# Performance work log

Hardware: AMD Instinct MI355X
Metric: run time of the kernel (lower is better)

Reference implementation:

```python
import jax, jax.numpy as jnp
import numpy as np

SDIM, EDIM, HID, DEPTH = 128, 128, 64, 4
CUTOFF, EPS = 5.0, 1e-6
N, E = 40000, 512000
MSG_IN = 2 * SDIM + EDIM + 2   # [s_src, s_dst, e, dist, ea_d]
SCAL_IN = SDIM + HID


def silu(x):
    return x * jax.nn.sigmoid(x)


def setup_inputs() -> dict:
    key = jax.random.key(0)
    ks = jax.random.split(key, 16)

    def w(k, shape, fan):
        return jax.random.normal(k, shape, jnp.float32) / np.float32(np.sqrt(fan))

    return {
        "s": jax.random.normal(ks[0], (N, SDIM), jnp.float32),
        "v": jax.random.normal(ks[1], (N, 3), jnp.float32),
        "e": jax.random.normal(ks[2], (E, EDIM), jnp.float32),
        "edge_index": jax.random.randint(ks[3], (2, E), 0, N),
        "ea_d": jax.random.uniform(ks[4], (E, 1), dtype=jnp.float32),
        "ea_r": jax.random.normal(ks[5], (E, 3), jnp.float32),
        "batch": jnp.zeros((N,), jnp.int32),
        "We1": w(ks[6], (DEPTH, MSG_IN, HID), MSG_IN),
        "be1": jnp.zeros((DEPTH, HID), jnp.float32),
        "We2": w(ks[7], (DEPTH, HID, HID), HID),
        "be2": jnp.zeros((DEPTH, HID), jnp.float32),
        "Weo": w(ks[8], (DEPTH, HID, EDIM), HID),
        "beo": jnp.zeros((DEPTH, EDIM), jnp.float32),
        "Wv": w(ks[9], (DEPTH, HID, 1), HID),
        "bv": jnp.zeros((DEPTH, 1), jnp.float32),
        "Ws1": w(ks[10], (DEPTH, SCAL_IN, HID), SCAL_IN),
        "bs1": jnp.zeros((DEPTH, HID), jnp.float32),
        "Ws2": w(ks[11], (DEPTH, HID, SDIM), HID),
        "bs2": jnp.zeros((DEPTH, SDIM), jnp.float32),
    }


def egnn_forward(s, v, e, src, dst, ea_d,
                 We1, be1, We2, be2, Weo, beo, Wv, bv, Ws1, bs1, Ws2, bs2):
    n = s.shape[0]
    ne = e.shape[0]
    # mean aggregation: per-destination degree (clamped to 1)
    deg = jax.ops.segment_sum(jnp.ones((ne, 1), s.dtype), dst, num_segments=n)
    deg = jnp.maximum(deg, 1.0)
    for i in range(DEPTH):
        rel = v[src] - v[dst]                                          # [E,3]
        dist = jnp.sqrt(jnp.sum(rel * rel, axis=-1, keepdims=True) + EPS)  # [E,1]
        cw = 0.5 * (jnp.cos(jnp.pi * dist / CUTOFF) + 1.0) * (dist < CUTOFF)
        h = jnp.concatenate([s[src], s[dst], e, dist, ea_d], axis=-1)  # [E,MSG_IN]
        m = silu(silu(h @ We1[i] + be1[i]) @ We2[i] + be2[i]) * cw      # [E,HID]
        e = e + m @ Weo[i] + beo[i]                                    # edge residual
        wv = m @ Wv[i] + bv[i]                                         # [E,1]
        v = v + jax.ops.segment_sum(rel * wv, dst, num_segments=n) / deg
        agg = jax.ops.segment_sum(m, dst, num_segments=n) / deg        # [N,HID]
        s = s + silu(jnp.concatenate([s, agg], axis=-1) @ Ws1[i] + bs1[i]) @ Ws2[i] + bs2[i]
    return s, v, e


def reference(s, v, e, edge_index, ea_d, ea_r, batch,
              We1, be1, We2, be2, Weo, beo, Wv, bv, Ws1, bs1, Ws2, bs2):
    del batch, ea_r  # unused in the enhanced (EGCL_Edge_Fast) path
    src, dst = edge_index[0], edge_index[1]
    return egnn_forward(s, v, e, src, dst, ea_d,
                        We1, be1, We2, be2, Weo, beo, Wv, bv, Ws1, bs1, Ws2, bs2)
```

## Files before the change

### kernel.cpp

```cpp
#include <hip/hip_runtime.h>
#include <math.h>

#define N_NODES 40000
#define N_EDGES 512000
#define SDIM 128
#define EDIM 128
#define HID 64
#define DEPTH 4
#define MSG_IN 386
#define SCAL_IN 192
#define CUTOFF 5.0f
#define EPS_D 1e-6f

#define TILE_M 16
#define EW 8
#define ETHREADS 512
#define EBLOCKS 256
#define TWAVES (EBLOCKS * EW)
#define NTILES (N_EDGES / TILE_M)
#define ATILES (N_NODES / TILE_M)
#define SCAN_B 1024
#define SCAN_NB ((N_NODES + SCAN_B - 1) / SCAN_B)

typedef __attribute__((ext_vector_type(8))) short short8;
typedef __attribute__((ext_vector_type(4))) float f32x4;
typedef unsigned long long ull;

__device__ __forceinline__ float silu_f(float x) { return x / (1.0f + __expf(-x)); }

__device__ __forceinline__ unsigned short f2b(float x) {
  union { __bf16 b; unsigned short u; } v;
  v.b = (__bf16)x;
  return v.u;
}

__device__ __forceinline__ float b2f(unsigned short u) {
  union { unsigned int u32; float f; } v; v.u32 = (unsigned int)u << 16; return v.f;
}

__device__ __forceinline__ short8 pack8(f32x4 lo, f32x4 hi) {
  union { unsigned short u[8]; short8 s; } pk;
  pk.u[0] = f2b(lo[0]); pk.u[1] = f2b(lo[1]); pk.u[2] = f2b(lo[2]); pk.u[3] = f2b(lo[3]);
  pk.u[4] = f2b(hi[0]); pk.u[5] = f2b(hi[1]); pk.u[6] = f2b(hi[2]); pk.u[7] = f2b(hi[3]);
  return pk.s;
}

__global__ __launch_bounds__(256) void k_zero(float* __restrict__ p, int n) {
  int i = blockIdx.x * 256 + threadIdx.x;
  int stride = gridDim.x * 256;
  for (; i < n; i += stride) p[i] = 0.0f;
}

__global__ __launch_bounds__(256) void k_cnt(const int* __restrict__ dst,
                                             int* __restrict__ cnt, int ne) {
  int i = blockIdx.x * 256 + threadIdx.x;
  if (i < ne) atomicAdd(&cnt[dst[i]], 1);
}

__global__ __launch_bounds__(256) void k_deginv_cnt(const int* __restrict__ cnt,
                                                    float* __restrict__ deginv, int n) {
  int i = blockIdx.x * 256 + threadIdx.x;
  if (i < n) deginv[i] = 1.0f / fmaxf((float)cnt[i], 1.0f);
}

__global__ __launch_bounds__(256) void k_scan1(const int* __restrict__ cnt,
                                               int* __restrict__ bstart,
                                               int* __restrict__ bsum, int n) {
  __shared__ int tmp[SCAN_B];
  const int base = blockIdx.x * SCAN_B;
  const int tid = threadIdx.x;
  for (int i = tid; i < SCAN_B; i += 256)
    tmp[i] = (base + i < n) ? cnt[base + i] : 0;
  __syncthreads();
  for (int off = 1; off < SCAN_B; off <<= 1) {
    int vals[4];
#pragma unroll
    for (int j = 0; j < 4; ++j) {
      const int i = tid + j * 256;
      vals[j] = (i >= off) ? tmp[i - off] : 0;
    }
    __syncthreads();
#pragma unroll
    for (int j = 0; j < 4; ++j) tmp[tid + j * 256] += vals[j];
    __syncthreads();
  }
  for (int i = tid; i < SCAN_B; i += 256)
    if (base + i < n) bstart[base + i] = tmp[i] - cnt[base + i];
  if (tid == 0) bsum[blockIdx.x] = tmp[SCAN_B - 1];
}

__global__ void k_scan2(int* __restrict__ bsum, int nb) {
  if (threadIdx.x == 0) {
    int run = 0;
    for (int i = 0; i < nb; ++i) { const int v = bsum[i]; bsum[i] = run; run += v; }
  }
}

__global__ __launch_bounds__(256) void k_scan3(int* __restrict__ bstart,
                                               const int* __restrict__ bsum,
                                               int* __restrict__ cursor, int n) {
  int i = blockIdx.x * 256 + threadIdx.x;
  if (i < n) {
    const int v = bstart[i] + bsum[i >> 10];
    bstart[i] = v;
    cursor[i] = v;
  }
}

__global__ __launch_bounds__(256) void k_scatter(const int* __restrict__ srcs,
                                                 const int* __restrict__ dsts,
                                                 const float* __restrict__ ead,
                                                 int* __restrict__ cursor,
                                                 int4* __restrict__ meta, int ne) {
  int i = blockIdx.x * 256 + threadIdx.x;
  if (i < ne) {
    const int d = dsts[i];
    const int pos = atomicAdd(&cursor[d], 1);
    int4 m;
    m.x = i; m.y = srcs[i]; m.z = d; m.w = __float_as_int(ead[i]);
    meta[pos] = m;
  }
}

__global__ __launch_bounds__(256) void k_prep(const int4* __restrict__ meta,
                                              const float* __restrict__ vbuf,
                                              float4* __restrict__ dynA,
                                              float* __restrict__ dynB, int ne) {
  int i = blockIdx.x * 256 + threadIdx.x;
  if (i < ne) {
    const int4 m = meta[i];
    const float dx = vbuf[m.y * 3 + 0] - vbuf[m.z * 3 + 0];
    const float dy = vbuf[m.y * 3 + 1] - vbuf[m.z * 3 + 1];
    const float dz = vbuf[m.y * 3 + 2] - vbuf[m.z * 3 + 2];
    const float dist = sqrtf(dx * dx + dy * dy + dz * dz + EPS_D);
    const float cwv = (dist < CUTOFF)
                          ? 0.5f * (__cosf((float)M_PI / CUTOFF * dist) + 1.0f)
                          : 0.0f;
    dynA[i] = make_float4(dx, dy, dz, dist);
    dynB[i] = cwv;
  }
}

__global__ __launch_bounds__(512, 2) void k_nodeA(
    const float* __restrict__ s, const float* __restrict__ W1,
    const float* __restrict__ be1_,
    unsigned short* __restrict__ SaP, unsigned short* __restrict__ SbP) {
  __shared__ __align__(16) unsigned short W1abt[64 * 264];
  __shared__ __align__(16) unsigned short snS[EW][16 * 136];
  const int tid = threadIdx.x, lane = tid & 63, w = tid >> 6;
  const int c = lane & 15, g = lane >> 4;
  for (int idx = tid; idx < 256 * 64; idx += 512) {
    const int k = idx >> 6, n = idx & 63;
    W1abt[n * 264 + k] = f2b(W1[idx]);
  }
  __syncthreads();
  float be1_l[4];
#pragma unroll
  for (int nt = 0; nt < 4; ++nt) be1_l[nt] = be1_[nt * 16 + c];
  unsigned short* sn = snS[w];

  for (int t = blockIdx.x * EW + w; t < ATILES; t += gridDim.x * EW) {
    const int n0 = t * TILE_M;
    const f32x4* sbase = (const f32x4*)(s + (size_t)n0 * SDIM);
#pragma unroll
    for (int i = 0; i < 4; ++i) {
      const int f = i * 128 + lane * 2;
      const f32x4 a = sbase[f], b = sbase[f + 1];
      *(short8*)&sn[(i * 4 + g) * 136 + c * 8] = pack8(a, b);
    }
    f32x4 aA[4], aB[4];
#pragma unroll
    for (int nt = 0; nt < 4; ++nt) {
      aA[nt] = f32x4{be1_l[nt], be1_l[nt], be1_l[nt], be1_l[nt]};
      aB[nt] = f32x4{0.f, 0.f, 0.f, 0.f};
    }
#pragma unroll
    for (int kc = 0; kc < 4; ++kc) {
      const short8 af = *(const short8*)&sn[c * 136 + kc * 32 + g * 8];
#pragma unroll
      for (int nt = 0; nt < 4; ++nt) {
        const short8 bfA = *(const short8*)&W1abt[(nt * 16 + c) * 264 + kc * 32 + g * 8];
        const short8 bfB = *(const short8*)&W1abt[(nt * 16 + c) * 264 + 128 + kc * 32 + g * 8];
        aA[nt] = __builtin_amdgcn_mfma_f32_16x16x32_bf16(af, bfA, aA[nt], 0, 0, 0);
        aB[nt] = __builtin_amdgcn_mfma_f32_16x16x32_bf16(af, bfB, aB[nt], 0, 0, 0);
      }
    }
#pragma unroll
    for (int r = 0; r < 4; ++r) {
      const size_t row = (size_t)(n0 + g * 4 + r);
      const ull pa = (ull)f2b(aA[0][r]) | ((ull)f2b(aA[1][r]) << 16)
                   | ((ull)f2b(aA[2][r]) << 32) | ((ull)f2b(aA[3][r]) << 48);
      const ull pb = (ull)f2b(aB[0][r]) | ((ull)f2b(aB[1][r]) << 16)
                   | ((ull)f2b(aB[2][r]) << 32) | ((ull)f2b(aB[3][r]) << 48);
      *(ull*)&SaP[row * 64 + c * 4] = pa;
      *(ull*)&SbP[row * 64 + c * 4] = pb;
    }
  }
}

__global__ __launch_bounds__(512, 2) void k_nodeC(
    const float* __restrict__ scur, float* __restrict__ s_dst,
    const float* __restrict__ vcur, float* __restrict__ v_dst,
    float* __restrict__ v_acc, float* __restrict__ agg,
    const float* __restrict__ deginv,
    const float* __restrict__ Ws1_, const float* __restrict__ bs1_,
    const float* __restrict__ Ws2_, const float* __restrict__ bs2_) {
  __shared__ __align__(16) unsigned short Ws1t[64 * 200];
  __shared__ __align__(16) unsigned short Ws2t[128 * 72];
  __shared__ __align__(16) unsigned short sAS[EW][16 * 200];
  __shared__ __align__(16) unsigned short hS[EW][16 * 72];
  __shared__ float dS[EW][16];
  const int tid = threadIdx.x, lane = tid & 63, w = tid >> 6;
  const int c = lane & 15, g = lane >> 4;
  for (int idx = tid; idx < 192 * 64; idx += 512) {
    const int k = idx >> 6, n = idx & 63;
    Ws1t[n * 200 + k] = f2b(Ws1_[idx]);
  }
  for (int idx = tid; idx < 64 * 128; idx += 512) {
    const int k = idx >> 7, n = idx & 127;
    Ws2t[n * 72 + k] = f2b(Ws2_[idx]);
  }
  __syncthreads();
  float bs1_l[4];
#pragma unroll
  for (int nt = 0; nt < 4; ++nt) bs1_l[nt] = bs1_[nt * 16 + c];
  f32x4 bs2V[2];
  bs2V[0] = *(const f32x4*)&bs2_[c * 4];
  bs2V[1] = *(const f32x4*)&bs2_[64 + c * 4];
  unsigned short* sA = sAS[w];
  unsigned short* hw = hS[w];
  float* ef = (float*)sAS[w];

  for (int t = blockIdx.x * EW + w; t < ATILES; t += gridDim.x * EW) {
    const int n0 = t * TILE_M;
    if (lane < 16) dS[w][lane] = deginv[n0 + lane];
    if (lane < 48) {
      const int i3 = n0 * 3 + lane;
      v_dst[i3] = vcur[i3] + v_acc[i3] * dS[w][lane / 3];
      v_acc[i3] = 0.0f;
    }
    const f32x4* sbase = (const f32x4*)(scur + (size_t)n0 * SDIM);
#pragma unroll
    for (int i = 0; i < 4; ++i) {
      const int f = i * 128 + lane * 2;
      const f32x4 a = sbase[f], b = sbase[f + 1];
      *(short8*)&sA[(i * 4 + g) * 200 + c * 8] = pack8(a, b);
    }
#pragma unroll
    for (int i = 0; i < 4; ++i) {
      const int row = i * 4 + g;
      float* ab = agg + (size_t)(n0 + row) * HID + c * 4;
      const f32x4 av = *(const f32x4*)ab;
      const float di = dS[w][row];
      union { unsigned short u[4]; ull ll; } pk4;
      pk4.u[0] = f2b(av[0] * di); pk4.u[1] = f2b(av[1] * di);
      pk4.u[2] = f2b(av[2] * di); pk4.u[3] = f2b(av[3] * di);
      *(ull*)&sA[row * 200 + 128 + c * 4] = pk4.ll;
      *(f32x4*)ab = f32x4{0.f, 0.f, 0.f, 0.f};
    }
    f32x4 acc[4];
#pragma unroll
    for (int nt = 0; nt < 4; ++nt)
      acc[nt] = f32x4{bs1_l[nt], bs1_l[nt], bs1_l[nt], bs1_l[nt]};
#pragma unroll
    for (int kc = 0; kc < 6; ++kc) {
      const short8 af = *(const short8*)&sA[c * 200 + kc * 32 + g * 8];
#pragma unroll
      for (int nt = 0; nt < 4; ++nt) {
        const short8 bf = *(const short8*)&Ws1t[(nt * 16 + c) * 200 + kc * 32 + g * 8];
        acc[nt] = __builtin_amdgcn_mfma_f32_16x16x32_bf16(af, bf, acc[nt], 0, 0, 0);
      }
    }
#pragma unroll
    for (int nt = 0; nt < 4; ++nt)
#pragma unroll
      for (int r = 0; r < 4; ++r)
        hw[(g * 4 + r) * 72 + nt * 16 + c] = f2b(silu_f(acc[nt][r]));
    f32x4 o[8];
#pragma unroll
    for (int nt = 0; nt < 8; ++nt) o[nt] = f32x4{0.f, 0.f, 0.f, 0.f};
#pragma unroll
    for (int kc = 0; kc < 2; ++kc) {
      const short8 am = *(const short8*)&hw[c * 72 + kc * 32 + g * 8];
#pragma unroll
      for (int nt = 0; nt < 8; ++nt) {
        const short8 bf = *(const short8*)&Ws2t[(nt * 16 + c) * 72 + kc * 32 + g * 8];
        o[nt] = __builtin_amdgcn_mfma_f32_16x16x32_bf16(am, bf, o[nt], 0, 0, 0);
      }
    }
#pragma unroll
    for (int h2 = 0; h2 < 2; ++h2) {
#pragma unroll
      for (int nt = 0; nt < 4; ++nt)
#pragma unroll
        for (int r = 0; r < 4; ++r)
          ef[(g * 4 + r) * 68 + nt * 16 + c] = o[h2 * 4 + nt][r];
#pragma unroll
      for (int q = 0; q < 4; ++q) {
        const int row = q * 4 + g;
        const f32x4 val = *(const f32x4*)&ef[row * 68 + c * 4];
        const size_t gi = (size_t)(n0 + row) * SDIM + h2 * 64 + c * 4;
        const f32x4 sres = *(const f32x4*)&scur[gi];
        *(f32x4*)&s_dst[gi] = val + bs2V[h2] + sres;
      }
    }
  }
}

template <typename TI, typename TO>
__global__ __launch_bounds__(ETHREADS, 1) void k_edge_mfma(
    const TI* __restrict__ e_src, TO* __restrict__ e_dst,
    const unsigned short* __restrict__ SaP, const unsigned short* __restrict__ SbP,
    const int4* __restrict__ meta, const float4* __restrict__ dynA,
    const float* __restrict__ dynB,
    const float* __restrict__ W1e,
    const float* __restrict__ w1d, const float* __restrict__ w1a,
    const float* __restrict__ We2_, const float* __restrict__ be2_,
    const float* __restrict__ Weo_, const float* __restrict__ beo_,
    const float* __restrict__ Wv_, const float* __restrict__ bv_,
    float* __restrict__ v_acc, float* __restrict__ agg) {
  constexpr bool IN16 = (sizeof(TI) == 2);
  constexpr bool OUT16 = (sizeof(TO) == 2);
  __shared__ __align__(16) unsigned short W1t[64 * 136];
  __shared__ __align__(16) unsigned short We2t[64 * 72];
  __shared__ __align__(16) unsigned short WeoT[128 * 72];
  __shared__ __align__(16) unsigned short eT[EW][TILE_M * 136];
  __shared__ __align__(16) float hm[EW][TILE_M * 68];
  __shared__ __align__(16) float sbufS[EW][2][160];

  const int tid = threadIdx.x;
  const int lane = tid & 63;
  const int w = tid >> 6;
  const int c = lane & 15;
  const int g = lane >> 4;

  for (int idx = tid; idx < 128 * 64; idx += ETHREADS) {
    const int k = idx >> 6, n = idx & 63;
    W1t[n * 136 + k] = f2b(W1e[idx]);
  }
  for (int idx = tid; idx < 64 * 64; idx += ETHREADS) {
    const int k = idx >> 6, n = idx & 63;
    We2t[n * 72 + k] = f2b(We2_[idx]);
  }
  for (int idx = tid; idx < 64 * 128; idx += ETHREADS) {
    const int k = idx >> 7, n = idx & 127;
    WeoT[n * 72 + k] = f2b(Weo_[idx]);
  }
  __syncthreads();

  float w1d_l[4], w1a_l[4], be2_l[4], Wv_l[4], beo_l[8];
#pragma unroll
  for (int nt = 0; nt < 4; ++nt) {
    w1d_l[nt] = w1d[nt * 16 + c];
    w1a_l[nt] = w1a[nt * 16 + c];
    be2_l[nt] = be2_[nt * 16 + c];
    Wv_l[nt]  = Wv_[nt * 16 + c];
  }
#pragma unroll
  for (int nt = 0; nt < 8; ++nt) beo_l[nt] = beo_[nt * 16 + c];
  const float bv0 = bv_[0];

  unsigned short* eTw = eT[w];
  float* hmw = hm[w];

  f32x4 eAf[8];
  short8 eAb[4];
  ull sabA[4], sabB[4];
  int4 metaR = {0, 0, 0, 0};
  float4 dynAR = {0.f, 0.f, 0.f, 0.f};
  float cwR = 0.f;

  const int t0 = blockIdx.x * EW + w;
  int cur = 0;

  {
    float* sb0 = &sbufS[w][0][0];
    int* sbi0 = (int*)sb0;
    if (lane < 16) {
      const int pos = t0 * TILE_M + lane;
      const int4 m = meta[pos];
      const float4 da = dynA[pos];
      const float cwv = dynB[pos];
      sb0[lane] = da.w; sb0[16 + lane] = cwv; sb0[32 + lane] = __int_as_float(m.w);
      sb0[48 + lane] = da.x; sb0[64 + lane] = da.y; sb0[80 + lane] = da.z;
      sbi0[96 + lane] = m.y; sbi0[112 + lane] = m.z; sbi0[128 + lane] = m.x;
    }
#pragma unroll
    for (int i = 0; i < 4; ++i) {
      const int er = sbi0[128 + i * 4 + g];
      if constexpr (IN16) {
        eAb[i] = *((const short8*)(e_src + (size_t)er * EDIM) + c);
      } else {
        const f32x4* eb = (const f32x4*)(e_src + (size_t)er * EDIM);
        eAf[i * 2] = eb[c * 2];
        eAf[i * 2 + 1] = eb[c * 2 + 1];
      }
    }
#pragma unroll
    for (int r = 0; r < 4; ++r) {
      sabA[r] = *(const ull*)&SaP[(size_t)sbi0[96 + g * 4 + r] * 64 + c * 4];
      sabB[r] = *(const ull*)&SbP[(size_t)sbi0[112 + g * 4 + r] * 64 + c * 4];
    }
    if (t0 + TWAVES < NTILES && lane < 16) {
      const int pos = (t0 + TWAVES) * TILE_M + lane;
      metaR = meta[pos]; dynAR = dynA[pos]; cwR = dynB[pos];
    }
  }

  for (int t = t0; t < NTILES; t += TWAVES) {
    const bool hasNext = (t + TWAVES) < NTILES;
    float* sbC = &sbufS[w][cur][0];
    int* sbiC = (int*)sbC;
    float* sbN = &sbufS[w][cur ^ 1][0];
    int* sbiN = (int*)sbN;

    if (hasNext && lane < 16) {
      sbN[lane] = dynAR.w; sbN[16 + lane] = cwR; sbN[32 + lane] = __int_as_float(metaR.w);
      sbN[48 + lane] = dynAR.x; sbN[64 + lane] = dynAR.y; sbN[80 + lane] = dynAR.z;
      sbiN[96 + lane] = metaR.y; sbiN[112 + lane] = metaR.z; sbiN[128 + lane] = metaR.x;
    }

#pragma unroll
    for (int i = 0; i < 4; ++i) {
      if constexpr (IN16)
        *(short8*)&eT[w][(i * 4 + g) * 136 + c * 8] = eAb[i];
      else
        *(short8*)&eT[w][(i * 4 + g) * 136 + c * 8] = pack8(eAf[i * 2], eAf[i * 2 + 1]);
    }

    float dist_r[4], cw_r[4], ea_r[4];
#pragma unroll
    for (int r = 0; r < 4; ++r) {
      const int row = g * 4 + r;
      dist_r[r] = sbC[row]; cw_r[r] = sbC[16 + row]; ea_r[r] = sbC[32 + row];
    }
    f32x4 acc[4];
#pragma unroll
    for (int nt = 0; nt < 4; ++nt)
#pragma unroll
      for (int r = 0; r < 4; ++r)
        acc[nt][r] = b2f((unsigned short)(sabA[r] >> (nt * 16)))
                   + b2f((unsigned short)(sabB[r] >> (nt * 16)))
                   + dist_r[r] * w1d_l[nt] + ea_r[r] * w1a_l[nt];

    if (hasNext) {
#pragma unroll
      for (int i = 0; i < 4; ++i) {
        const int er = sbiN[128 + i * 4 + g];
        if constexpr (IN16) {
          eAb[i] = *((const short8*)(e_src + (size_t)er * EDIM) + c);
        } else {
          const f32x4* eb = (const f32x4*)(e_src + (size_t)er * EDIM);
          eAf[i * 2] = eb[c * 2];
          eAf[i * 2 + 1] = eb[c * 2 + 1];
        }
      }
#pragma unroll
      for (int r = 0; r < 4; ++r) {
        sabA[r] = *(const ull*)&SaP[(size_t)sbiN[96 + g * 4 + r] * 64 + c * 4];
        sabB[r] = *(const ull*)&SbP[(size_t)sbiN[112 + g * 4 + r] * 64 + c * 4];
      }
      if (t + 2 * TWAVES < NTILES && lane < 16) {
        const int pos = (t + 2 * TWAVES) * TILE_M + lane;
        metaR = meta[pos]; dynAR = dynA[pos]; cwR = dynB[pos];
      }
    }

#pragma unroll
    for (int kc = 0; kc < 4; ++kc) {
      const short8 af = *(const short8*)&eTw[c * 136 + kc * 32 + g * 8];
#pragma unroll
      for (int nt = 0; nt < 4; ++nt) {
        const short8 bf = *(const short8*)&W1t[(nt * 16 + c) * 136 + kc * 32 + g * 8];
        acc[nt] = __builtin_amdgcn_mfma_f32_16x16x32_bf16(af, bf, acc[nt], 0, 0, 0);
      }
    }
#pragma unroll
    for (int nt = 0; nt < 4; ++nt)
#pragma unroll
      for (int r = 0; r < 4; ++r)
        hmw[(g * 4 + r) * 68 + nt * 16 + c] = silu_f(acc[nt][r]);

    f32x4 acc2[4];
#pragma unroll
    for (int nt = 0; nt < 4; ++nt)
      acc2[nt] = f32x4{be2_l[nt], be2_l[nt], be2_l[nt], be2_l[nt]};
#pragma unroll
    for (int kc = 0; kc < 2; ++kc) {
      const f32x4 lo = *(const f32x4*)&hmw[c * 68 + kc * 32 + g * 8];
      const f32x4 hi = *(const f32x4*)&hmw[c * 68 + kc * 32 + g * 8 + 4];
      const short8 am = pack8(lo, hi);
#pragma unroll
      for (int nt = 0; nt < 4; ++nt) {
        const short8 bf = *(const short8*)&We2t[(nt * 16 + c) * 72 + kc * 32 + g * 8];
        acc2[nt] = __builtin_amdgcn_mfma_f32_16x16x32_bf16(am, bf, acc2[nt], 0, 0, 0);
      }
    }
    float mval[4][4];
#pragma unroll
    for (int nt = 0; nt < 4; ++nt)
#pragma unroll
      for (int r = 0; r < 4; ++r)
        mval[nt][r] = silu_f(acc2[nt][r]) * cw_r[r];

#pragma unroll
    for (int nt = 0; nt < 4; ++nt)
#pragma unroll
      for (int r = 0; r < 4; ++r)
        hmw[(g * 4 + r) * 68 + nt * 16 + c] = mval[nt][r];

#pragma unroll
    for (int r = 0; r < 4; ++r) {
      float s = mval[0][r] * Wv_l[0];
#pragma unroll
      for (int nt = 1; nt < 4; ++nt) s = fmaf(mval[nt][r], Wv_l[nt], s);
      s += __shfl_xor(s, 1); s += __shfl_xor(s, 2);
      s += __shfl_xor(s, 4); s += __shfl_xor(s, 8);
      if (c == 0) sbC[144 + g * 4 + r] = s + bv0;
    }

    {
      float accum = 0.f;
#pragma unroll
      for (int row = 0; row < 16; ++row) {
        accum += hmw[row * 68 + lane];
        const int dd = sbiC[112 + row];
        const bool cut = (row == 15) || (sbiC[113 + row] != dd);
        if (cut) {
          atomicAdd(&agg[(size_t)dd * HID + lane], accum);
          accum = 0.f;
        }
      }
    }
    if (lane < 3) {
      float accum = 0.f;
#pragma unroll
      for (int row = 0; row < 16; ++row) {
        accum = fmaf(sbC[48 + 16 * lane + row], sbC[144 + row], accum);
        const int dd = sbiC[112 + row];
        const bool cut = (row == 15) || (sbiC[113 + row] != dd);
        if (cut) {
          atomicAdd(&v_acc[(size_t)dd * 3 + lane], accum);
          accum = 0.f;
        }
      }
    }

    f32x4 oacc[8];
#pragma unroll
    for (int nt = 0; nt < 8; ++nt)
      oacc[nt] = f32x4{beo_l[nt], beo_l[nt], beo_l[nt], beo_l[nt]};
#pragma unroll
    for (int kc = 0; kc < 2; ++kc) {
      const f32x4 lo = *(const f32x4*)&hmw[c * 68 + kc * 32 + g * 8];
      const f32x4 hi = *(const f32x4*)&hmw[c * 68 + kc * 32 + g * 8 + 4];
      const short8 am = pack8(lo, hi);
#pragma unroll
      for (int nt = 0; nt < 8; ++nt) {
        const short8 bf = *(const short8*)&WeoT[(nt * 16 + c) * 72 + kc * 32 + g * 8];
        oacc[nt] = __builtin_amdgcn_mfma_f32_16x16x32_bf16(am, bf, oacc[nt], 0, 0, 0);
      }
    }

#pragma unroll
    for (int h2 = 0; h2 < 2; ++h2) {
#pragma unroll
      for (int nt = 0; nt < 4; ++nt)
#pragma unroll
        for (int r = 0; r < 4; ++r)
          hmw[(g * 4 + r) * 68 + nt * 16 + c] = oacc[h2 * 4 + nt][r];
#pragma unroll
      for (int q = 0; q < 4; ++q) {
        const int row = q * 4 + g;
        const int er = sbiC[128 + row];
        const f32x4 val = *(const f32x4*)&hmw[row * 68 + c * 4];
        f32x4 old;
        if constexpr (IN16) {
#pragma unroll
          for (int j = 0; j < 4; ++j)
            old[j] = b2f(eTw[row * 136 + h2 * 64 + c * 4 + j]);
        } else {
          old = *(const f32x4*)&e_src[(size_t)er * EDIM + h2 * 64 + c * 4];
        }
        const f32x4 sum = val + old;
        if constexpr (OUT16) {
          union { unsigned short u[4]; ull ll; } pk4;
          pk4.u[0] = f2b(sum[0]); pk4.u[1] = f2b(sum[1]);
          pk4.u[2] = f2b(sum[2]); pk4.u[3] = f2b(sum[3]);
          *(ull*)&e_dst[(size_t)er * EDIM + h2 * 64 + c * 4] = pk4.ll;
        } else {
          *(f32x4*)&e_dst[(size_t)er * EDIM + h2 * 64 + c * 4] = sum;
        }
      }
    }
    cur ^= 1;
  }
}

extern "C" void kernel_launch(void* const* d_in, const int* in_sizes, int n_in,
                              void* d_out, int out_size, void* d_ws, size_t ws_size,
                              hipStream_t stream) {
  const float* s_in = (const float*)d_in[0];
  const float* v_in = (const float*)d_in[1];
  const float* e_in = (const float*)d_in[2];
  const int*   eidx = (const int*)d_in[3];
  const float* ead  = (const float*)d_in[4];
  const float* We1 = (const float*)d_in[7];
  const float* be1 = (const float*)d_in[8];
  const float* We2 = (const float*)d_in[9];
  const float* be2 = (const float*)d_in[10];
  const float* Weo = (const float*)d_in[11];
  const float* beo = (const float*)d_in[12];
  const float* Wv  = (const float*)d_in[13];
  const float* bv  = (const float*)d_in[14];
  const float* Ws1 = (const float*)d_in[15];
  const float* bs1 = (const float*)d_in[16];
  const float* Ws2 = (const float*)d_in[17];
  const float* bs2 = (const float*)d_in[18];

  float* out_s = (float*)d_out;
  float* out_v = out_s + (size_t)N_NODES * SDIM;
  float* out_e = out_v + (size_t)N_NODES * 3;

  float* ws     = (float*)d_ws;
  float* deginv = ws;
  float* v_acc  = deginv + N_NODES;
  float* agg    = v_acc + (size_t)3 * N_NODES;
  unsigned short* SaP = (unsigned short*)(agg + (size_t)64 * N_NODES);
  unsigned short* SbP = SaP + (size_t)64 * N_NODES;
  int* cnt     = (int*)(SbP + (size_t)64 * N_NODES);
  int* bstart  = cnt + N_NODES;
  int* cursor  = bstart + N_NODES;
  int* bsum    = cursor + N_NODES;
  int4* meta   = (int4*)(bsum + 64);
  float4* dynA = (float4*)(meta + N_EDGES);
  float* dynB  = (float*)(dynA + N_EDGES);
  unsigned short* eb16 = (unsigned short*)(dynB + N_EDGES);

  const size_t NEED = (size_t)((char*)(eb16 + (size_t)N_EDGES * EDIM) - (char*)d_ws);
  const bool u16e = (ws_size >= NEED);

  const int* srcs = eidx;
  const int* dsts = eidx + N_EDGES;

  hipLaunchKernelGGL(k_zero, dim3(512), dim3(256), 0, stream,
                     deginv, (1 + 3 + 64) * N_NODES);
  hipLaunchKernelGGL(k_zero, dim3(64), dim3(256), 0, stream,
                     (float*)cnt, N_NODES);
  hipLaunchKernelGGL(k_cnt, dim3((N_EDGES + 255) / 256), dim3(256), 0, stream,
                     dsts, cnt, N_EDGES);
  hipLaunchKernelGGL(k_deginv_cnt, dim3((N_NODES + 255) / 256), dim3(256), 0, stream,
                     cnt, deginv, N_NODES);
  hipLaunchKernelGGL(k_scan1, dim3(SCAN_NB), dim3(256), 0, stream,
                     cnt, bstart, bsum, N_NODES);
  hipLaunchKernelGGL(k_scan2, dim3(1), dim3(64), 0, stream, bsum, SCAN_NB);
  hipLaunchKernelGGL(k_scan3, dim3((N_NODES + 255) / 256), dim3(256), 0, stream,
                     bstart, bsum, cursor, N_NODES);
  hipLaunchKernelGGL(k_scatter, dim3((N_EDGES + 255) / 256), dim3(256), 0, stream,
                     srcs, dsts, ead, cursor, meta, N_EDGES);

  hipLaunchKernelGGL(k_nodeA, dim3(512), dim3(512), 0, stream,
                     s_in, We1, be1, SaP, SbP);

  for (int i = 0; i < DEPTH; ++i) {
    const float* W1i = We1 + (size_t)i * MSG_IN * HID;
    hipLaunchKernelGGL(k_prep, dim3((N_EDGES + 255) / 256), dim3(256), 0, stream,
                       meta, (i == 0) ? v_in : out_v, dynA, dynB, N_EDGES);
#define EDGE_ARGS                                                              \
      SaP, SbP, meta, dynA, dynB,                                              \
      W1i + 256 * HID, W1i + 384 * HID, W1i + 385 * HID,                       \
      We2 + (size_t)i * HID * HID, be2 + i * HID,                              \
      Weo + (size_t)i * HID * EDIM, beo + i * EDIM,                            \
      Wv + i * HID, bv + i, v_acc, agg
    if (u16e) {
      if (i == 0)
        k_edge_mfma<float, unsigned short>
            <<<dim3(EBLOCKS), dim3(ETHREADS), 0, stream>>>(e_in, eb16, EDGE_ARGS);
      else if (i == DEPTH - 1)
        k_edge_mfma<unsigned short, float>
            <<<dim3(EBLOCKS), dim3(ETHREADS), 0, stream>>>(eb16, out_e, EDGE_ARGS);
      else
        k_edge_mfma<unsigned short, unsigned short>
            <<<dim3(EBLOCKS), dim3(ETHREADS), 0, stream>>>(eb16, eb16, EDGE_ARGS);
    } else {
      k_edge_mfma<float, float>
          <<<dim3(EBLOCKS), dim3(ETHREADS), 0, stream>>>(
              (i == 0) ? e_in : out_e, out_e, EDGE_ARGS);
    }
#undef EDGE_ARGS
    hipLaunchKernelGGL(k_nodeC, dim3(EBLOCKS), dim3(512), 0, stream,
                       (i == 0) ? s_in : out_s, out_s,
                       (i == 0) ? v_in : out_v, out_v,
                       v_acc, agg, deginv,
                       Ws1 + (size_t)i * SCAL_IN * HID, bs1 + i * HID,
                       Ws2 + (size_t)i * HID * SDIM, bs2 + i * SDIM);
    if (i + 1 < DEPTH)
      hipLaunchKernelGGL(k_nodeA, dim3(512), dim3(512), 0, stream,
                         out_s, We1 + (size_t)(i + 1) * MSG_IN * HID,
                         be1 + (i + 1) * HID, SaP, SbP);
  }
}
```

Measured before the change: 742.6 us.

## Fuse next-layer node projection into nodeC and keep bf16 edge tiles in registers

Folds the next layer's node-side We1 projections (Sa/Sb) into k_nodeC, so the updated s tile is reused from shared memory and the separate k_nodeA launch and its re-read of s disappear. The s output epilogue now writes per-element directly instead of staging through shared memory. In the bf16 edge kernel, e rows are loaded straight into MFMA A-operand layout in registers, which skips the LDS transpose. The residual add then re-reads the old e from global. This adds LDS use and registers in nodeC, and the per-element stores are less coalesced.

```diff
diff --git a/kernel.cpp b/kernel.cpp
--- a/kernel.cpp
+++ b/kernel.cpp
@@ -204,9 +204,13 @@
     float* __restrict__ v_acc, float* __restrict__ agg,
     const float* __restrict__ deginv,
     const float* __restrict__ Ws1_, const float* __restrict__ bs1_,
-    const float* __restrict__ Ws2_, const float* __restrict__ bs2_) {
+    const float* __restrict__ Ws2_, const float* __restrict__ bs2_,
+    const float* __restrict__ W1n, const float* __restrict__ be1n,
+    unsigned short* __restrict__ SaP, unsigned short* __restrict__ SbP,
+    int doA) {
   __shared__ __align__(16) unsigned short Ws1t[64 * 200];
   __shared__ __align__(16) unsigned short Ws2t[128 * 72];
+  __shared__ __align__(16) unsigned short W1abt[64 * 264];
   __shared__ __align__(16) unsigned short sAS[EW][16 * 200];
   __shared__ __align__(16) unsigned short hS[EW][16 * 72];
   __shared__ float dS[EW][16];
@@ -220,16 +224,22 @@
     const int k = idx >> 7, n = idx & 127;
     Ws2t[n * 72 + k] = f2b(Ws2_[idx]);
   }
+  if (doA) {
+    for (int idx = tid; idx < 256 * 64; idx += 512) {
+      const int k = idx >> 6, n = idx & 63;
+      W1abt[n * 264 + k] = f2b(W1n[idx]);
+    }
+  }
   __syncthreads();
-  float bs1_l[4];
+  float bs1_l[4], bs2_l[8], be1_l[4];
 #pragma unroll
   for (int nt = 0; nt < 4; ++nt) bs1_l[nt] = bs1_[nt * 16 + c];
-  f32x4 bs2V[2];
-  bs2V[0] = *(const f32x4*)&bs2_[c * 4];
-  bs2V[1] = *(const f32x4*)&bs2_[64 + c * 4];
+#pragma unroll
+  for (int j = 0; j < 8; ++j) bs2_l[j] = bs2_[j * 16 + c];
+#pragma unroll
+  for (int nt = 0; nt < 4; ++nt) be1_l[nt] = doA ? be1n[nt * 16 + c] : 0.0f;
   unsigned short* sA = sAS[w];
   unsigned short* hw = hS[w];
-  float* ef = (float*)sAS[w];
 
   for (int t = blockIdx.x * EW + w; t < ATILES; t += gridDim.x * EW) {
     const int n0 = t * TILE_M;
@@ -289,19 +299,44 @@
       }
     }
 #pragma unroll
-    for (int h2 = 0; h2 < 2; ++h2) {
-#pragma unroll
-      for (int nt = 0; nt < 4; ++nt)
-#pragma unroll
-        for (int r = 0; r < 4; ++r)
-          ef[(g * 4 + r) * 68 + nt * 16 + c] = o[h2 * 4 + nt][r];
-#pragma unroll
-      for (int q = 0; q < 4; ++q) {
-        const int row = q * 4 + g;
-        const f32x4 val = *(const f32x4*)&ef[row * 68 + c * 4];
-        const size_t gi = (size_t)(n0 + row) * SDIM + h2 * 64 + c * 4;
-        const f32x4 sres = *(const f32x4*)&scur[gi];
-        *(f32x4*)&s_dst[gi] = val + bs2V[h2] + sres;
+    for (int j = 0; j < 8; ++j) {
+      const int col = j * 16 + c;
+#pragma unroll
+      for (int r = 0; r < 4; ++r) {
+        const int row = g * 4 + r;
+        const size_t gi = (size_t)(n0 + row) * SDIM + col;
+        const float sum = o[j][r] + bs2_l[j] + scur[gi];
+        s_dst[gi] = sum;
+        if (doA) sA[row * 200 + col] = f2b(sum);
+      }
+    }
+    if (doA) {
+      f32x4 aA[4], aB[4];
+#pragma unroll
+      for (int nt = 0; nt < 4; ++nt) {
+        aA[nt] = f32x4{be1_l[nt], be1_l[nt], be1_l[nt], be1_l[nt]};
+        aB[nt] = f32x4{0.f, 0.f, 0.f, 0.f};
+      }
+#pragma unroll
+      for (int kc = 0; kc < 4; ++kc) {
+        const short8 af = *(const short8*)&sA[c * 200 + kc * 32 + g * 8];
+#pragma unroll
+        for (int nt = 0; nt < 4; ++nt) {
+          const short8 bfA = *(const short8*)&W1abt[(nt * 16 + c) * 264 + kc * 32 + g * 8];
+          const short8 bfB = *(const short8*)&W1abt[(nt * 16 + c) * 264 + 128 + kc * 32 + g * 8];
+          aA[nt] = __builtin_amdgcn_mfma_f32_16x16x32_bf16(af, bfA, aA[nt], 0, 0, 0);
+          aB[nt] = __builtin_amdgcn_mfma_f32_16x16x32_bf16(af, bfB, aB[nt], 0, 0, 0);
+        }
+      }
+#pragma unroll
+      for (int r = 0; r < 4; ++r) {
+        const size_t row = (size_t)(n0 + g * 4 + r);
+        const ull pa = (ull)f2b(aA[0][r]) | ((ull)f2b(aA[1][r]) << 16)
+                     | ((ull)f2b(aA[2][r]) << 32) | ((ull)f2b(aA[3][r]) << 48);
+        const ull pb = (ull)f2b(aB[0][r]) | ((ull)f2b(aB[1][r]) << 16)
+                     | ((ull)f2b(aB[2][r]) << 32) | ((ull)f2b(aB[3][r]) << 48);
+        *(ull*)&SaP[row * 64 + c * 4] = pa;
+        *(ull*)&SbP[row * 64 + c * 4] = pb;
       }
     }
   }
@@ -385,12 +420,16 @@
       sb0[48 + lane] = da.x; sb0[64 + lane] = da.y; sb0[80 + lane] = da.z;
       sbi0[96 + lane] = m.y; sbi0[112 + lane] = m.z; sbi0[128 + lane] = m.x;
     }
-#pragma unroll
-    for (int i = 0; i < 4; ++i) {
-      const int er = sbi0[128 + i * 4 + g];
-      if constexpr (IN16) {
-        eAb[i] = *((const short8*)(e_src + (size_t)er * EDIM) + c);
-      } else {
+    if constexpr (IN16) {
+      const int erc = sbi0[128 + c];
+      const TI* rowp = e_src + (size_t)erc * EDIM;
+#pragma unroll
+      for (int kc = 0; kc < 4; ++kc)
+        eAb[kc] = *(const short8*)(rowp + kc * 32 + g * 8);
+    } else {
+#pragma unroll
+      for (int i = 0; i < 4; ++i) {
+        const int er = sbi0[128 + i * 4 + g];
         const f32x4* eb = (const f32x4*)(e_src + (size_t)er * EDIM);
         eAf[i * 2] = eb[c * 2];
         eAf[i * 2 + 1] = eb[c * 2 + 1];
@@ -420,11 +459,13 @@
       sbiN[96 + lane] = metaR.y; sbiN[112 + lane] = metaR.z; sbiN[128 + lane] = metaR.x;
     }
 
-#pragma unroll
-    for (int i = 0; i < 4; ++i) {
-      if constexpr (IN16)
-        *(short8*)&eT[w][(i * 4 + g) * 136 + c * 8] = eAb[i];
-      else
+    short8 afT[4];
+    if constexpr (IN16) {
+#pragma unroll
+      for (int kc = 0; kc < 4; ++kc) afT[kc] = eAb[kc];
+    } else {
+#pragma unroll
+      for (int i = 0; i < 4; ++i)
         *(short8*)&eT[w][(i * 4 + g) * 136 + c * 8] = pack8(eAf[i * 2], eAf[i * 2 + 1]);
     }
 
@@ -444,12 +485,16 @@
                    + dist_r[r] * w1d_l[nt] + ea_r[r] * w1a_l[nt];
 
     if (hasNext) {
-#pragma unroll
-      for (int i = 0; i < 4; ++i) {
-        const int er = sbiN[128 + i * 4 + g];
-        if constexpr (IN16) {
-          eAb[i] = *((const short8*)(e_src + (size_t)er * EDIM) + c);
-        } else {
+      if constexpr (IN16) {
+        const int erc = sbiN[128 + c];
+        const TI* rowp = e_src + (size_t)erc * EDIM;
+#pragma unroll
+        for (int kc = 0; kc < 4; ++kc)
+          eAb[kc] = *(const short8*)(rowp + kc * 32 + g * 8);
+      } else {
+#pragma unroll
+        for (int i = 0; i < 4; ++i) {
+          const int er = sbiN[128 + i * 4 + g];
           const f32x4* eb = (const f32x4*)(e_src + (size_t)er * EDIM);
           eAf[i * 2] = eb[c * 2];
           eAf[i * 2 + 1] = eb[c * 2 + 1];
@@ -468,7 +513,11 @@
 
 #pragma unroll
     for (int kc = 0; kc < 4; ++kc) {
-      const short8 af = *(const short8*)&eTw[c * 136 + kc * 32 + g * 8];
+      short8 af;
+      if constexpr (IN16)
+        af = afT[kc];
+      else
+        af = *(const short8*)&eTw[c * 136 + kc * 32 + g * 8];
 #pragma unroll
       for (int nt = 0; nt < 4; ++nt) {
         const short8 bf = *(const short8*)&W1t[(nt * 16 + c) * 136 + kc * 32 + g * 8];
@@ -576,9 +625,10 @@
         const f32x4 val = *(const f32x4*)&hmw[row * 68 + c * 4];
         f32x4 old;
         if constexpr (IN16) {
+          const ull ov = *(const ull*)&e_src[(size_t)er * EDIM + h2 * 64 + c * 4];
 #pragma unroll
           for (int j = 0; j < 4; ++j)
-            old[j] = b2f(eTw[row * 136 + h2 * 64 + c * 4 + j]);
+            old[j] = b2f((unsigned short)(ov >> (16 * j)));
         } else {
           old = *(const f32x4*)&e_src[(size_t)er * EDIM + h2 * 64 + c * 4];
         }
@@ -664,6 +714,7 @@
 
   for (int i = 0; i < DEPTH; ++i) {
     const float* W1i = We1 + (size_t)i * MSG_IN * HID;
+    const int dn = (i + 1 < DEPTH) ? i + 1 : i;
     hipLaunchKernelGGL(k_prep, dim3((N_EDGES + 255) / 256), dim3(256), 0, stream,
                        meta, (i == 0) ? v_in : out_v, dynA, dynB, N_EDGES);
 #define EDGE_ARGS                                                              \
@@ -693,10 +744,8 @@
                        (i == 0) ? v_in : out_v, out_v,
                        v_acc, agg, deginv,
                        Ws1 + (size_t)i * SCAL_IN * HID, bs1 + i * HID,
-                       Ws2 + (size_t)i * HID * SDIM, bs2 + i * SDIM);
-    if (i + 1 < DEPTH)
-      hipLaunchKernelGGL(k_nodeA, dim3(512), dim3(512), 0, stream,
-                         out_s, We1 + (size_t)(i + 1) * MSG_IN * HID,
-                         be1 + (i + 1) * HID, SaP, SbP);
-  }
-}
+                       Ws2 + (size_t)i * HID * SDIM, bs2 + i * SDIM,
+                       We1 + (size_t)dn * MSG_IN * HID, be1 + dn * HID,
+                       SaP, SbP, (i + 1 < DEPTH) ? 1 : 0);
+  }
+}
```

New measurement: 762.1 us. 2.6% more time.
